# Kernel tuning notes

Hardware: AMD Instinct MI355X
Metric: run time of the kernel (lower is better)

The kernel has to match this reference:

```python
import jax, jax.numpy as jnp
import numpy as np

B, N, C, H = 2, 2048, 1024, 16
HD = C // H  # head dim = 64


def setup_inputs() -> dict:
    key = jax.random.key(0)
    kq, kk, kv, km = jax.random.split(key, 4)
    q = jax.random.normal(kq, (B, N, C), dtype=jnp.float32)
    k = jax.random.normal(kk, (B, N, C), dtype=jnp.float32)
    v = jax.random.normal(kv, (B, N, C), dtype=jnp.float32)
    mask = jax.random.randint(km, (B, 1, N, N), 0, 2, dtype=jnp.int32)
    return {"q": q, "k": k, "v": v, "mask": mask}


def reference(q, k, v, mask):
    b, n, c = q.shape
    # (B, N, C) -> (B, H, N, HD)
    qh = q.reshape(b, n, H, HD).transpose(0, 2, 1, 3)
    kh = k.reshape(b, n, H, HD).transpose(0, 2, 1, 3)
    vh = v.reshape(b, n, H, HD).transpose(0, 2, 1, 3)
    scale = 1.0 / jnp.sqrt(jnp.float32(HD))
    # scores: (B, H, N, N)
    scores = jnp.einsum("bhqd,bhkd->bhqk", qh, kh) * scale
    scores = jnp.where(mask == 0, jnp.float32(-1e9), scores)
    probs = jax.nn.softmax(scores, axis=-1)
    atten = jnp.einsum("bhqk,bhkd->bhqd", probs, vh)
    # (B, H, N, HD) -> (B, N, C)
    return atten.transpose(0, 2, 1, 3).reshape(b, n, c)
```

## Files before the change

### kernel.cpp

```cpp
#include <hip/hip_runtime.h>
#include <hip/hip_bf16.h>

#define B_ 2
#define N_ 2048
#define C_ 1024
#define H_ 16
#define HD_ 64

#define KT 64
#define NT (N_ / KT)
#define TILE_E 4096
#define PSTR 72
#define NW 8
#define QB 128

#define QBM 128

typedef short s16x8 __attribute__((ext_vector_type(8)));
typedef short s16x4 __attribute__((ext_vector_type(4)));
typedef float f32x4 __attribute__((ext_vector_type(4)));
typedef float f32x16 __attribute__((ext_vector_type(16)));

__device__ __forceinline__ s16x8 cvt8(float4 a, float4 b) {
    union { s16x8 v; __hip_bfloat162 h[4]; } u;
    u.h[0] = __float22bfloat162_rn(float2{a.x, a.y});
    u.h[1] = __float22bfloat162_rn(float2{a.z, a.w});
    u.h[2] = __float22bfloat162_rn(float2{b.x, b.y});
    u.h[3] = __float22bfloat162_rn(float2{b.z, b.w});
    return u.v;
}

__device__ __forceinline__ void gll16(const void* g, void* l) {
    __builtin_amdgcn_global_load_lds(
        (const __attribute__((address_space(1))) unsigned*)g,
        (__attribute__((address_space(3))) unsigned*)l, 16, 0, 0);
}

__global__ __launch_bounds__(256)
void pack_mask(const int* __restrict__ M, unsigned long long* __restrict__ bits) {
    const int gw   = (blockIdx.x * 256 + threadIdx.x) >> 6;
    const int lane = threadIdx.x & 63;
#pragma unroll
    for (int it = 0; it < 16; ++it) {
        const size_t wi = (size_t)gw * 16 + it;
        unsigned long long bal = __ballot(M[wi * 64 + lane] != 0);
        if (lane == 0) bits[wi] = bal;
    }
}

__global__ __launch_bounds__(256)
void prepass(const int* __restrict__ M, const float* __restrict__ K,
             const float* __restrict__ V, unsigned long long* __restrict__ bits,
             ushort* __restrict__ Kw, ushort* __restrict__ Vw) {
    const int bid = blockIdx.x;
    const int tid = threadIdx.x;
    if (bid < 2048) {
        const int gt = bid * 256 + tid;
        const int4* src = (const int4*)M + (size_t)gt * 4;
        unsigned r = 0;
#pragma unroll
        for (int c = 0; c < 4; ++c) {
            const int4 m4 = src[c];
            r |= (m4.x != 0 ? 1u : 0u) << (c * 4 + 0);
            r |= (m4.y != 0 ? 1u : 0u) << (c * 4 + 1);
            r |= (m4.z != 0 ? 1u : 0u) << (c * 4 + 2);
            r |= (m4.w != 0 ? 1u : 0u) << (c * 4 + 3);
        }
        ((ushort*)bits)[gt] = (ushort)r;
    } else if (bid < 4096) {
        const int gt = (bid - 2048) * 256 + tid;
        const int b  = gt >> 18;
        const int h  = (gt >> 14) & 15;
        const int n  = (gt >> 3) & 2047;
        const int db = gt & 7;
        const size_t src = (size_t)(b * N_ + n) * C_ + h * 64 + db * 8;
        float4 f0 = *(const float4*)(K + src);
        float4 f1 = *(const float4*)(K + src + 4);
        const int key = n & 63, kt = n >> 6;
        const int p = (key & 32) | ((key & 4) << 2) | ((key & 16) >> 1)
                    | ((key & 8) >> 1) | (key & 3);
        ushort* dst = Kw + (size_t)((b * H_ + h) * NT + kt) * TILE_E
                         + p * 64 + ((db ^ (p & 7)) * 8);
        *(s16x8*)dst = cvt8(f0, f1);
    } else {
        const int gt  = (bid - 4096) * 256 + tid;
        const int b   = gt >> 16;
        const int h   = (gt >> 12) & 15;
        const int kt  = (gt >> 7) & 31;
        const int kb4 = (gt >> 3) & 15;
        const int db  = gt & 7;
        const int key0 = kb4 * 4;
        float f[4][8];
#pragma unroll
        for (int i = 0; i < 4; ++i) {
            const size_t src = (size_t)(b * N_ + kt * 64 + key0 + i) * C_ + h * 64 + db * 8;
            *(float4*)&f[i][0] = *(const float4*)(V + src);
            *(float4*)&f[i][4] = *(const float4*)(V + src + 4);
        }
        ushort* tb = Vw + (size_t)((b * H_ + h) * NT + kt) * TILE_E;
#pragma unroll
        for (int j = 0; j < 8; ++j) {
            const int d = db * 8 + j;
            union { s16x4 v; __hip_bfloat162 h2[2]; } u;
            u.h2[0] = __float22bfloat162_rn(float2{f[0][j], f[1][j]});
            u.h2[1] = __float22bfloat162_rn(float2{f[2][j], f[3][j]});
            *(s16x4*)(tb + d * 64 + (((key0 >> 3) ^ (d & 7)) * 8) + (key0 & 7)) = u.v;
        }
    }
}

__global__ __launch_bounds__(256)
void mha_fwd(const float* __restrict__ Q, const ushort* __restrict__ Kw,
             const ushort* __restrict__ Vw, const unsigned* __restrict__ bits,
             float* __restrict__ O) {
    __shared__ ushort Kl[2][TILE_E];
    __shared__ ushort Vt[2][TILE_E];

    const int sid = blockIdx.x;
    const int jj  = sid >> 3;
    const int hb  = ((sid & 7) << 2) | (jj & 3);
    const int qt  = jj >> 2;
    const int h   = hb & 15;
    const int b   = hb >> 4;

    const int tid  = threadIdx.x;
    const int w    = tid >> 6;
    const int lane = tid & 63;
    const int rl   = lane & 31;
    const int hh   = lane >> 5;
    const int e3   = rl & 7;

    const size_t head_off = (size_t)b * N_ * C_ + (size_t)h * HD_;
    const int qb = qt * QBM + w * 32;

    const float qs = 0.125f * 1.44269504088896f;
    const size_t qoff = head_off + (size_t)(qb + rl) * C_ + hh * 8;
    s16x8 qa[4];
#pragma unroll
    for (int i = 0; i < 4; ++i) {
        float4 a = *(const float4*)(Q + qoff + i * 16);
        float4 c = *(const float4*)(Q + qoff + i * 16 + 4);
        a.x*=qs; a.y*=qs; a.z*=qs; a.w*=qs;
        c.x*=qs; c.y*=qs; c.z*=qs; c.w*=qs;
        qa[i] = cvt8(a, c);
    }

    s16x8 onesb;
#pragma unroll
    for (int i = 0; i < 8; ++i) onesb[i] = (short)0x3F80;

    f32x16 acc0, acc1, sum;
#pragma unroll
    for (int j = 0; j < 16; ++j) { acc0[j] = 0.f; acc1[j] = 0.f; sum[j] = 0.f; }

    const size_t tilebase = (size_t)((b * H_ + h) * NT) * TILE_E;
    const ushort* Kg = Kw + tilebase + (size_t)tid * 8;
    const ushort* Vg = Vw + tilebase + (size_t)tid * 8;

    const unsigned* mq = bits + ((size_t)b * N_ + qb + rl) * (N_ / 32);

    gll16(Kg,        &Kl[0][w * 512]);
    gll16(Kg + 2048, &Kl[0][w * 512 + 2048]);
    gll16(Vg,        &Vt[0][w * 512]);
    gll16(Vg + 2048, &Vt[0][w * 512 + 2048]);
    const ushort* Kg_pf = Kg + TILE_E;
    const ushort* Vg_pf = Vg + TILE_E;

    uint4 mw = *(const uint4*)mq;  mq += 4;

    for (int kt2 = 0; kt2 < NT; kt2 += 2) {
        const bool pf1 = (kt2 + 2 < NT);
        uint4 mw_nxt = mw;
        if (pf1) { mw_nxt = *(const uint4*)mq; }
        mq += 4;
#pragma unroll
        for (int u = 0; u < 2; ++u) {
            __syncthreads();
            if (u == 0 || pf1) {
                gll16(Kg_pf,        &Kl[1 - u][w * 512]);
                gll16(Kg_pf + 2048, &Kl[1 - u][w * 512 + 2048]);
                gll16(Vg_pf,        &Vt[1 - u][w * 512]);
                gll16(Vg_pf + 2048, &Vt[1 - u][w * 512 + 2048]);
                Kg_pf += TILE_E;  Vg_pf += TILE_E;
            }

            f32x16 z0, z1;
#pragma unroll
            for (int j = 0; j < 16; ++j) { z0[j] = 0.f; z1[j] = 0.f; }
            __builtin_amdgcn_s_setprio(1);
#pragma unroll
            for (int i = 0; i < 4; ++i) {
                const int cb = ((i << 1) | hh) ^ e3;
                s16x8 k0 = *(const s16x8*)(&Kl[u][rl * 64 + (cb << 3)]);
                s16x8 k1 = *(const s16x8*)(&Kl[u][(rl + 32) * 64 + (cb << 3)]);
                z0 = __builtin_amdgcn_mfma_f32_32x32x16_bf16(k0, qa[i], z0, 0, 0, 0);
                z1 = __builtin_amdgcn_mfma_f32_32x32x16_bf16(k1, qa[i], z1, 0, 0, 0);
            }
            __builtin_amdgcn_s_setprio(0);

            const unsigned g0 = (u ? mw.z : mw.x) >> (hh * 8);
            const unsigned g1 = (u ? mw.w : mw.y) >> (hh * 8);
            s16x8 pa[4];
            auto soft = [&](const f32x16& z, unsigned wg, s16x8& fA, s16x8& fB) {
                float p[16];
#pragma unroll
                for (int R = 0; R < 4; ++R) {
                    const int base = ((R & 1) << 4) + ((R >> 1) << 2);
#pragma unroll
                    for (int r = 0; r < 4; ++r)
                        p[4 * R + r] = __builtin_amdgcn_exp2f(
                            ((wg >> (base + r)) & 1u) ? z[4 * R + r] : -1e9f);
                }
                union { s16x8 v; __hip_bfloat162 h2[4]; } uA, uB;
                uA.h2[0] = __float22bfloat162_rn(float2{p[0], p[1]});
                uA.h2[1] = __float22bfloat162_rn(float2{p[2], p[3]});
                uA.h2[2] = __float22bfloat162_rn(float2{p[8], p[9]});
                uA.h2[3] = __float22bfloat162_rn(float2{p[10], p[11]});
                uB.h2[0] = __float22bfloat162_rn(float2{p[4], p[5]});
                uB.h2[1] = __float22bfloat162_rn(float2{p[6], p[7]});
                uB.h2[2] = __float22bfloat162_rn(float2{p[12], p[13]});
                uB.h2[3] = __float22bfloat162_rn(float2{p[14], p[15]});
                fA = uA.v;  fB = uB.v;
            };
            soft(z0, g0, pa[0], pa[1]);
            soft(z1, g1, pa[2], pa[3]);

            __builtin_amdgcn_s_setprio(1);
#pragma unroll
            for (int i = 0; i < 4; ++i) {
                const int cb = ((i << 1) | hh) ^ e3;
                s16x8 v0 = *(const s16x8*)(&Vt[u][rl * 64 + (cb << 3)]);
                s16x8 v1 = *(const s16x8*)(&Vt[u][(rl + 32) * 64 + (cb << 3)]);
                acc0 = __builtin_amdgcn_mfma_f32_32x32x16_bf16(pa[i], v0, acc0, 0, 0, 0);
                acc1 = __builtin_amdgcn_mfma_f32_32x32x16_bf16(pa[i], v1, acc1, 0, 0, 0);
                sum  = __builtin_amdgcn_mfma_f32_32x32x16_bf16(pa[i], onesb, sum, 0, 0, 0);
            }
            __builtin_amdgcn_s_setprio(0);
        }
        mw = mw_nxt;
    }

#pragma unroll
    for (int reg = 0; reg < 16; ++reg) {
        const int qrow = qb + (reg & 3) + ((reg >> 2) << 3) + (hh << 2);
        const float inv = 1.0f / sum[reg];
        const size_t ob = head_off + (size_t)qrow * C_;
        O[ob + rl]      = acc0[reg] * inv;
        O[ob + rl + 32] = acc1[reg] * inv;
    }
}

#define KSTR 72
#define VSTR 72
__global__ __launch_bounds__(512, 4)
void mha_fwd_fb(const float* __restrict__ Q, const float* __restrict__ K,
                const float* __restrict__ V, const unsigned* __restrict__ bits,
                float* __restrict__ O) {
    __shared__ ushort Kl[2][KT * KSTR];
    __shared__ ushort Vt[2][HD_ * VSTR];
    __shared__ ushort Pl[NW][16 * PSTR];
    const int qt = blockIdx.x, h = blockIdx.y, b = blockIdx.z, tid = threadIdx.x;
    const int w = tid >> 6, lane = tid & 63, l16 = lane & 15, quad = lane >> 4;
    const size_t head_off = (size_t)b * N_ * C_ + (size_t)h * HD_;
    const int qb = qt * QB + w * 16;
    const float qs = 0.125f * 1.44269504088896f;
    const size_t qoff = head_off + (size_t)(qb + l16) * C_ + quad * 8;
    float4 q0 = *(const float4*)(Q + qoff);
    float4 q1 = *(const float4*)(Q + qoff + 4);
    float4 q2 = *(const float4*)(Q + qoff + 32);
    float4 q3 = *(const float4*)(Q + qoff + 36);
    q0.x*=qs; q0.y*=qs; q0.z*=qs; q0.w*=qs;
    q1.x*=qs; q1.y*=qs; q1.z*=qs; q1.w*=qs;
    q2.x*=qs; q2.y*=qs; q2.z*=qs; q2.w*=qs;
    q3.x*=qs; q3.y*=qs; q3.z*=qs; q3.w*=qs;
    const s16x8 qa0 = cvt8(q0, q1);
    const s16x8 qa1 = cvt8(q2, q3);
    f32x4 acc[4];
#pragma unroll
    for (int c = 0; c < 4; ++c) acc[c] = f32x4{0.f, 0.f, 0.f, 0.f};
    float lsum = 0.f;
    const int skey = tid >> 3, sd0 = (tid & 7) * 8;
    const int kp = tid >> 4, vd0 = (tid & 15) * 4;
    const int vcol = 2 * (kp & 3) + ((((kp >> 2) ^ (vd0 >> 3)) & 7) << 3);
    const unsigned* brow = bits + ((size_t)b * N_ + qb + l16) * (N_ / 32);
    const float SHIFT = 16.0f;
    {
        const size_t kbase = head_off + (size_t)skey * C_ + sd0;
        float4 kA = *(const float4*)(K + kbase);
        float4 kB = *(const float4*)(K + kbase + 4);
        *(s16x8*)(&Kl[0][skey * KSTR + sd0]) = cvt8(kA, kB);
        const size_t vbase = head_off + (size_t)(2 * kp) * C_ + vd0;
        float4 vA = *(const float4*)(V + vbase);
        float4 vB = *(const float4*)(V + vbase + C_);
        const float* ap = (const float*)&vA;
        const float* bp = (const float*)&vB;
#pragma unroll
        for (int i = 0; i < 4; ++i) {
            __hip_bfloat162 pr = __float22bfloat162_rn(float2{ap[i], bp[i]});
            *(unsigned*)(&Vt[0][(vd0 + i) * VSTR + vcol]) = *(unsigned*)&pr;
        }
    }
    for (int kt = 0; kt < NT; ++kt) {
        const int cur = kt & 1;
        float4 kA, kB, vA, vB;
        const bool has_next = (kt + 1 < NT);
        if (has_next) {
            const size_t kbase = head_off + (size_t)((kt + 1) * KT + skey) * C_ + sd0;
            kA = *(const float4*)(K + kbase);
            kB = *(const float4*)(K + kbase + 4);
            const size_t vbase = head_off + (size_t)((kt + 1) * KT + 2 * kp) * C_ + vd0;
            vA = *(const float4*)(V + vbase);
            vB = *(const float4*)(V + vbase + C_);
        }
        const unsigned w0 = brow[2 * kt];
        const unsigned w1 = brow[2 * kt + 1];
        __syncthreads();
        f32x4 s[4];
#pragma unroll
        for (int t = 0; t < 4; ++t) {
            s16x8 kb0 = *(const s16x8*)(&Kl[cur][(t * 16 + l16) * KSTR + quad * 8]);
            s16x8 kb1 = *(const s16x8*)(&Kl[cur][(t * 16 + l16) * KSTR + quad * 8 + 32]);
            f32x4 z = {0.f, 0.f, 0.f, 0.f};
            z = __builtin_amdgcn_mfma_f32_16x16x32_bf16(kb0, qa0, z, 0, 0, 0);
            z = __builtin_amdgcn_mfma_f32_16x16x32_bf16(kb1, qa1, z, 0, 0, 0);
            s[t] = z;
        }
        const unsigned a0 = w0 >> (quad * 4);
        const unsigned a1 = w1 >> (quad * 4);
#pragma unroll
        for (int t = 0; t < 4; ++t) {
            const unsigned aw = (t < 2) ? a0 : a1;
            const int sh = (t & 1) * 16;
            float p0 = exp2f((((aw >> (sh + 0)) & 1u) ? s[t][0] : -1e9f) - SHIFT);
            float p1 = exp2f((((aw >> (sh + 1)) & 1u) ? s[t][1] : -1e9f) - SHIFT);
            float p2 = exp2f((((aw >> (sh + 2)) & 1u) ? s[t][2] : -1e9f) - SHIFT);
            float p3 = exp2f((((aw >> (sh + 3)) & 1u) ? s[t][3] : -1e9f) - SHIFT);
            lsum += (p0 + p1) + (p2 + p3);
            union { s16x4 v; __hip_bfloat162 h2[2]; } uu;
            uu.h2[0] = __float22bfloat162_rn(float2{p0, p1});
            uu.h2[1] = __float22bfloat162_rn(float2{p2, p3});
            *(s16x4*)(&Pl[w][l16 * PSTR + t * 16 + quad * 4]) = uu.v;
        }
#pragma unroll
        for (int half = 0; half < 2; ++half) {
            s16x8 pa = *(const s16x8*)(&Pl[w][l16 * PSTR + half * 32 + quad * 8]);
#pragma unroll
            for (int c = 0; c < 4; ++c) {
                const int dr = c * 16 + l16;
                const int blk = (half * 4 + quad) ^ ((dr >> 3) & 7);
                s16x8 vb = *(const s16x8*)(&Vt[cur][dr * VSTR + blk * 8]);
                acc[c] = __builtin_amdgcn_mfma_f32_16x16x32_bf16(pa, vb, acc[c], 0, 0, 0);
            }
        }
        if (has_next) {
            *(s16x8*)(&Kl[1 - cur][skey * KSTR + sd0]) = cvt8(kA, kB);
            const float* ap = (const float*)&vA;
            const float* bp = (const float*)&vB;
#pragma unroll
            for (int i = 0; i < 4; ++i) {
                __hip_bfloat162 pr = __float22bfloat162_rn(float2{ap[i], bp[i]});
                *(unsigned*)(&Vt[1 - cur][(vd0 + i) * VSTR + vcol]) = *(unsigned*)&pr;
            }
        }
    }
    lsum += __shfl_xor(lsum, 16);
    lsum += __shfl_xor(lsum, 32);
#pragma unroll
    for (int r = 0; r < 4; ++r) {
        const float inv = 1.0f / __shfl(lsum, quad * 4 + r);
        const size_t obase = head_off + (size_t)(qb + quad * 4 + r) * C_;
        O[obase + l16]      = acc[0][r] * inv;
        O[obase + l16 + 16] = acc[1][r] * inv;
        O[obase + l16 + 32] = acc[2][r] * inv;
        O[obase + l16 + 48] = acc[3][r] * inv;
    }
}

extern "C" void kernel_launch(void* const* d_in, const int* in_sizes, int n_in,
                              void* d_out, int out_size, void* d_ws, size_t ws_size,
                              hipStream_t stream) {
    const float* q = (const float*)d_in[0];
    const float* k = (const float*)d_in[1];
    const float* v = (const float*)d_in[2];
    const int*   m = (const int*)d_in[3];
    float*       o = (float*)d_out;

    const size_t BITS_BYTES = (size_t)B_ * N_ * N_ / 8;
    const size_t KV_BYTES   = (size_t)B_ * H_ * N_ * HD_ * 2;
    const size_t NEED       = BITS_BYTES + 2 * KV_BYTES;

    unsigned long long* bits = (unsigned long long*)d_ws;

    if (ws_size >= NEED) {
        ushort* kw = (ushort*)((char*)d_ws + BITS_BYTES);
        ushort* vw = (ushort*)((char*)d_ws + BITS_BYTES + KV_BYTES);
        hipLaunchKernelGGL(prepass, dim3(4608), dim3(256), 0, stream,
                           m, k, v, bits, kw, vw);
        hipLaunchKernelGGL(mha_fwd, dim3(512), dim3(256), 0, stream,
                           q, kw, vw, (const unsigned*)bits, o);
    } else {
        hipLaunchKernelGGL(pack_mask, dim3(2048), dim3(256), 0, stream, m, bits);
        dim3 grid(N_ / QB, H_, B_);
        hipLaunchKernelGGL(mha_fwd_fb, grid, dim3(512), 0, stream,
                           q, k, v, (const unsigned*)bits, o);
    }
}
```

Baseline: 167.5 us.

## Process two key tiles per barrier with double-buffered pairs of K/V tiles

The main loop now loads two K/V tiles (a 128-key chunk) into each of two LDS buffers and runs one __syncthreads per pair instead of one per tile. Both QK^T MFMA groups run before the softmax and PV steps, so the second tile's score MFMAs can overlap the first tile's exp work. This halves barrier count and lengthens the prefetch distance. In exchange LDS use doubles to 64 KB per block and four score accumulators raise register pressure, which may lower occupancy.

Measured after the change: 166.8 us. About the same (-0.4%).

```diff
diff --git a/kernel.cpp b/kernel.cpp
--- a/kernel.cpp
+++ b/kernel.cpp
@@ -113,8 +113,8 @@
 void mha_fwd(const float* __restrict__ Q, const ushort* __restrict__ Kw,
              const ushort* __restrict__ Vw, const unsigned* __restrict__ bits,
              float* __restrict__ O) {
-    __shared__ ushort Kl[2][TILE_E];
-    __shared__ ushort Vt[2][TILE_E];
+    __shared__ ushort Kl[2][2][TILE_E];
+    __shared__ ushort Vt[2][2][TILE_E];
 
     const int sid = blockIdx.x;
     const int jj  = sid >> 3;
@@ -159,84 +159,118 @@
 
     const unsigned* mq = bits + ((size_t)b * N_ + qb + rl) * (N_ / 32);
 
-    gll16(Kg,        &Kl[0][w * 512]);
-    gll16(Kg + 2048, &Kl[0][w * 512 + 2048]);
-    gll16(Vg,        &Vt[0][w * 512]);
-    gll16(Vg + 2048, &Vt[0][w * 512 + 2048]);
-    const ushort* Kg_pf = Kg + TILE_E;
-    const ushort* Vg_pf = Vg + TILE_E;
+#pragma unroll
+    for (int uu = 0; uu < 2; ++uu) {
+        gll16(Kg + uu * TILE_E,        &Kl[0][uu][w * 512]);
+        gll16(Kg + uu * TILE_E + 2048, &Kl[0][uu][w * 512 + 2048]);
+        gll16(Vg + uu * TILE_E,        &Vt[0][uu][w * 512]);
+        gll16(Vg + uu * TILE_E + 2048, &Vt[0][uu][w * 512 + 2048]);
+    }
+    const ushort* Kg_pf = Kg + 2 * TILE_E;
+    const ushort* Vg_pf = Vg + 2 * TILE_E;
 
     uint4 mw = *(const uint4*)mq;  mq += 4;
 
+    auto soft = [&](const f32x16& z, unsigned wg, s16x8& fA, s16x8& fB) {
+        float p[16];
+#pragma unroll
+        for (int R = 0; R < 4; ++R) {
+            const int base = ((R & 1) << 4) + ((R >> 1) << 2);
+#pragma unroll
+            for (int r = 0; r < 4; ++r)
+                p[4 * R + r] = __builtin_amdgcn_exp2f(
+                    ((wg >> (base + r)) & 1u) ? z[4 * R + r] : -1e9f);
+        }
+        union { s16x8 v; __hip_bfloat162 h2[4]; } uA, uB;
+        uA.h2[0] = __float22bfloat162_rn(float2{p[0], p[1]});
+        uA.h2[1] = __float22bfloat162_rn(float2{p[2], p[3]});
+        uA.h2[2] = __float22bfloat162_rn(float2{p[8], p[9]});
+        uA.h2[3] = __float22bfloat162_rn(float2{p[10], p[11]});
+        uB.h2[0] = __float22bfloat162_rn(float2{p[4], p[5]});
+        uB.h2[1] = __float22bfloat162_rn(float2{p[6], p[7]});
+        uB.h2[2] = __float22bfloat162_rn(float2{p[12], p[13]});
+        uB.h2[3] = __float22bfloat162_rn(float2{p[14], p[15]});
+        fA = uA.v;  fB = uB.v;
+    };
+
     for (int kt2 = 0; kt2 < NT; kt2 += 2) {
-        const bool pf1 = (kt2 + 2 < NT);
+        const int buf = (kt2 >> 1) & 1;
+        const bool pf = (kt2 + 2 < NT);
         uint4 mw_nxt = mw;
-        if (pf1) { mw_nxt = *(const uint4*)mq; }
+        if (pf) { mw_nxt = *(const uint4*)mq; }
         mq += 4;
-#pragma unroll
-        for (int u = 0; u < 2; ++u) {
-            __syncthreads();
-            if (u == 0 || pf1) {
-                gll16(Kg_pf,        &Kl[1 - u][w * 512]);
-                gll16(Kg_pf + 2048, &Kl[1 - u][w * 512 + 2048]);
-                gll16(Vg_pf,        &Vt[1 - u][w * 512]);
-                gll16(Vg_pf + 2048, &Vt[1 - u][w * 512 + 2048]);
-                Kg_pf += TILE_E;  Vg_pf += TILE_E;
+
+        __syncthreads();
+        if (pf) {
+#pragma unroll
+            for (int uu = 0; uu < 2; ++uu) {
+                gll16(Kg_pf + uu * TILE_E,        &Kl[buf ^ 1][uu][w * 512]);
+                gll16(Kg_pf + uu * TILE_E + 2048, &Kl[buf ^ 1][uu][w * 512 + 2048]);
+                gll16(Vg_pf + uu * TILE_E,        &Vt[buf ^ 1][uu][w * 512]);
+                gll16(Vg_pf + uu * TILE_E + 2048, &Vt[buf ^ 1][uu][w * 512 + 2048]);
             }
-
-            f32x16 z0, z1;
-#pragma unroll
-            for (int j = 0; j < 16; ++j) { z0[j] = 0.f; z1[j] = 0.f; }
-            __builtin_amdgcn_s_setprio(1);
-#pragma unroll
-            for (int i = 0; i < 4; ++i) {
-                const int cb = ((i << 1) | hh) ^ e3;
-                s16x8 k0 = *(const s16x8*)(&Kl[u][rl * 64 + (cb << 3)]);
-                s16x8 k1 = *(const s16x8*)(&Kl[u][(rl + 32) * 64 + (cb << 3)]);
-                z0 = __builtin_amdgcn_mfma_f32_32x32x16_bf16(k0, qa[i], z0, 0, 0, 0);
-                z1 = __builtin_amdgcn_mfma_f32_32x32x16_bf16(k1, qa[i], z1, 0, 0, 0);
-            }
-            __builtin_amdgcn_s_setprio(0);
-
-            const unsigned g0 = (u ? mw.z : mw.x) >> (hh * 8);
-            const unsigned g1 = (u ? mw.w : mw.y) >> (hh * 8);
-            s16x8 pa[4];
-            auto soft = [&](const f32x16& z, unsigned wg, s16x8& fA, s16x8& fB) {
-                float p[16];
-#pragma unroll
-                for (int R = 0; R < 4; ++R) {
-                    const int base = ((R & 1) << 4) + ((R >> 1) << 2);
-#pragma unroll
-                    for (int r = 0; r < 4; ++r)
-                        p[4 * R + r] = __builtin_amdgcn_exp2f(
-                            ((wg >> (base + r)) & 1u) ? z[4 * R + r] : -1e9f);
-                }
-                union { s16x8 v; __hip_bfloat162 h2[4]; } uA, uB;
-                uA.h2[0] = __float22bfloat162_rn(float2{p[0], p[1]});
-                uA.h2[1] = __float22bfloat162_rn(float2{p[2], p[3]});
-                uA.h2[2] = __float22bfloat162_rn(float2{p[8], p[9]});
-                uA.h2[3] = __float22bfloat162_rn(float2{p[10], p[11]});
-                uB.h2[0] = __float22bfloat162_rn(float2{p[4], p[5]});
-                uB.h2[1] = __float22bfloat162_rn(float2{p[6], p[7]});
-                uB.h2[2] = __float22bfloat162_rn(float2{p[12], p[13]});
-                uB.h2[3] = __float22bfloat162_rn(float2{p[14], p[15]});
-                fA = uA.v;  fB = uB.v;
-            };
-            soft(z0, g0, pa[0], pa[1]);
-            soft(z1, g1, pa[2], pa[3]);
-
-            __builtin_amdgcn_s_setprio(1);
-#pragma unroll
-            for (int i = 0; i < 4; ++i) {
-                const int cb = ((i << 1) | hh) ^ e3;
-                s16x8 v0 = *(const s16x8*)(&Vt[u][rl * 64 + (cb << 3)]);
-                s16x8 v1 = *(const s16x8*)(&Vt[u][(rl + 32) * 64 + (cb << 3)]);
-                acc0 = __builtin_amdgcn_mfma_f32_32x32x16_bf16(pa[i], v0, acc0, 0, 0, 0);
-                acc1 = __builtin_amdgcn_mfma_f32_32x32x16_bf16(pa[i], v1, acc1, 0, 0, 0);
-                sum  = __builtin_amdgcn_mfma_f32_32x32x16_bf16(pa[i], onesb, sum, 0, 0, 0);
-            }
-            __builtin_amdgcn_s_setprio(0);
-        }
+            Kg_pf += 2 * TILE_E;  Vg_pf += 2 * TILE_E;
+        }
+
+        const ushort* K0 = &Kl[buf][0][0];
+        const ushort* K1 = &Kl[buf][1][0];
+        const ushort* V0 = &Vt[buf][0][0];
+        const ushort* V1 = &Vt[buf][1][0];
+
+        f32x16 z0, z1, z2, z3;
+#pragma unroll
+        for (int j = 0; j < 16; ++j) { z0[j]=0.f; z1[j]=0.f; z2[j]=0.f; z3[j]=0.f; }
+        __builtin_amdgcn_s_setprio(1);
+#pragma unroll
+        for (int i = 0; i < 4; ++i) {
+            const int cb = ((i << 1) | hh) ^ e3;
+            s16x8 k0 = *(const s16x8*)(K0 + rl * 64 + (cb << 3));
+            s16x8 k1 = *(const s16x8*)(K0 + (rl + 32) * 64 + (cb << 3));
+            z0 = __builtin_amdgcn_mfma_f32_32x32x16_bf16(k0, qa[i], z0, 0, 0, 0);
+            z1 = __builtin_amdgcn_mfma_f32_32x32x16_bf16(k1, qa[i], z1, 0, 0, 0);
+        }
+#pragma unroll
+        for (int i = 0; i < 4; ++i) {
+            const int cb = ((i << 1) | hh) ^ e3;
+            s16x8 k0 = *(const s16x8*)(K1 + rl * 64 + (cb << 3));
+            s16x8 k1 = *(const s16x8*)(K1 + (rl + 32) * 64 + (cb << 3));
+            z2 = __builtin_amdgcn_mfma_f32_32x32x16_bf16(k0, qa[i], z2, 0, 0, 0);
+            z3 = __builtin_amdgcn_mfma_f32_32x32x16_bf16(k1, qa[i], z3, 0, 0, 0);
+        }
+        __builtin_amdgcn_s_setprio(0);
+
+        s16x8 pa0[4];
+        soft(z0, mw.x >> (hh * 8), pa0[0], pa0[1]);
+        soft(z1, mw.y >> (hh * 8), pa0[2], pa0[3]);
+
+        __builtin_amdgcn_s_setprio(1);
+#pragma unroll
+        for (int i = 0; i < 4; ++i) {
+            const int cb = ((i << 1) | hh) ^ e3;
+            s16x8 v0 = *(const s16x8*)(V0 + rl * 64 + (cb << 3));
+            s16x8 v1 = *(const s16x8*)(V0 + (rl + 32) * 64 + (cb << 3));
+            acc0 = __builtin_amdgcn_mfma_f32_32x32x16_bf16(pa0[i], v0, acc0, 0, 0, 0);
+            acc1 = __builtin_amdgcn_mfma_f32_32x32x16_bf16(pa0[i], v1, acc1, 0, 0, 0);
+            sum  = __builtin_amdgcn_mfma_f32_32x32x16_bf16(pa0[i], onesb, sum, 0, 0, 0);
+        }
+        __builtin_amdgcn_s_setprio(0);
+
+        s16x8 pa1[4];
+        soft(z2, mw.z >> (hh * 8), pa1[0], pa1[1]);
+        soft(z3, mw.w >> (hh * 8), pa1[2], pa1[3]);
+
+        __builtin_amdgcn_s_setprio(1);
+#pragma unroll
+        for (int i = 0; i < 4; ++i) {
+            const int cb = ((i << 1) | hh) ^ e3;
+            s16x8 v0 = *(const s16x8*)(V1 + rl * 64 + (cb << 3));
+            s16x8 v1 = *(const s16x8*)(V1 + (rl + 32) * 64 + (cb << 3));
+            acc0 = __builtin_amdgcn_mfma_f32_32x32x16_bf16(pa1[i], v0, acc0, 0, 0, 0);
+            acc1 = __builtin_amdgcn_mfma_f32_32x32x16_bf16(pa1[i], v1, acc1, 0, 0, 0);
+            sum  = __builtin_amdgcn_mfma_f32_32x32x16_bf16(pa1[i], onesb, sum, 0, 0, 0);
+        }
+        __builtin_amdgcn_s_setprio(0);
+
         mw = mw_nxt;
     }
 
```

## Split attention key range across two blocks with a combine kernel

Applied to the files above, without the earlier changes.

Adds a split-K (flash-decoding style) path: each query tile's key sequence is split into two halves handled by separate blocks (1024 blocks instead of 512), each writing unnormalized partial accumulators and row sums to workspace. A new combine kernel sums the two partials and normalizes. The aim is more parallelism and occupancy on the many CUs. The cost is extra global traffic for the fp32 partials and a third kernel launch. The path relies on no max subtraction, since scores are unnormalized exp2 values, so the partials can simply be added.

Measured after the change: 180.0 us. +7.5%, slower.

```diff
diff --git a/kernel.cpp b/kernel.cpp
--- a/kernel.cpp
+++ b/kernel.cpp
@@ -9,6 +9,7 @@
 
 #define KT 64
 #define NT (N_ / KT)
+#define NTS (NT / 2)
 #define TILE_E 4096
 #define PSTR 72
 #define NW 8
@@ -107,6 +108,178 @@
             *(s16x4*)(tb + d * 64 + (((key0 >> 3) ^ (d & 7)) * 8) + (key0 & 7)) = u.v;
         }
     }
+}
+
+__global__ __launch_bounds__(256, 4)
+void mha_fwd_sk(const float* __restrict__ Q, const ushort* __restrict__ Kw,
+                const ushort* __restrict__ Vw, const unsigned* __restrict__ bits,
+                float* __restrict__ accw, float* __restrict__ sumw) {
+    __shared__ ushort Kl[2][TILE_E];
+    __shared__ ushort Vt[2][TILE_E];
+
+    const int sid  = blockIdx.x;
+    const int xcd  = sid & 7;
+    const int rest = sid >> 3;
+    const int hb   = (xcd << 2) | (rest & 3);
+    const int qt   = (rest >> 2) & 15;
+    const int sp   = rest >> 6;
+    const int h    = hb & 15;
+    const int b    = hb >> 4;
+
+    const int tid  = threadIdx.x;
+    const int w    = tid >> 6;
+    const int lane = tid & 63;
+    const int rl   = lane & 31;
+    const int hh   = lane >> 5;
+    const int e3   = rl & 7;
+
+    const size_t head_off = (size_t)b * N_ * C_ + (size_t)h * HD_;
+    const int qb = qt * QBM + w * 32;
+
+    const float qs = 0.125f * 1.44269504088896f;
+    const size_t qoff = head_off + (size_t)(qb + rl) * C_ + hh * 8;
+    s16x8 qa[4];
+#pragma unroll
+    for (int i = 0; i < 4; ++i) {
+        float4 a = *(const float4*)(Q + qoff + i * 16);
+        float4 c = *(const float4*)(Q + qoff + i * 16 + 4);
+        a.x*=qs; a.y*=qs; a.z*=qs; a.w*=qs;
+        c.x*=qs; c.y*=qs; c.z*=qs; c.w*=qs;
+        qa[i] = cvt8(a, c);
+    }
+
+    s16x8 onesb;
+#pragma unroll
+    for (int i = 0; i < 8; ++i) onesb[i] = (short)0x3F80;
+
+    f32x16 acc0, acc1, sum;
+#pragma unroll
+    for (int j = 0; j < 16; ++j) { acc0[j] = 0.f; acc1[j] = 0.f; sum[j] = 0.f; }
+
+    const size_t tilebase = (size_t)((b * H_ + h) * NT + sp * NTS) * TILE_E;
+    const ushort* Kg = Kw + tilebase + (size_t)tid * 8;
+    const ushort* Vg = Vw + tilebase + (size_t)tid * 8;
+
+    const unsigned* mq = bits + ((size_t)b * N_ + qb + rl) * (N_ / 32) + sp * (NTS * 2);
+
+    gll16(Kg,        &Kl[0][w * 512]);
+    gll16(Kg + 2048, &Kl[0][w * 512 + 2048]);
+    gll16(Vg,        &Vt[0][w * 512]);
+    gll16(Vg + 2048, &Vt[0][w * 512 + 2048]);
+    const ushort* Kg_pf = Kg + TILE_E;
+    const ushort* Vg_pf = Vg + TILE_E;
+
+    uint4 mw = *(const uint4*)mq;  mq += 4;
+
+    auto soft = [&](const f32x16& z, unsigned wg, s16x8& fA, s16x8& fB) {
+        float p[16];
+#pragma unroll
+        for (int R = 0; R < 4; ++R) {
+            const int base = ((R & 1) << 4) + ((R >> 1) << 2);
+#pragma unroll
+            for (int r = 0; r < 4; ++r) {
+                const int bit = base + r;
+                const float e = __builtin_amdgcn_exp2f(z[4 * R + r]);
+                const unsigned m = (unsigned)((int)(wg << (31 - bit)) >> 31);
+                p[4 * R + r] = __uint_as_float(__float_as_uint(e) & m);
+            }
+        }
+        union { s16x8 v; __hip_bfloat162 h2[4]; } uA, uB;
+        uA.h2[0] = __float22bfloat162_rn(float2{p[0], p[1]});
+        uA.h2[1] = __float22bfloat162_rn(float2{p[2], p[3]});
+        uA.h2[2] = __float22bfloat162_rn(float2{p[8], p[9]});
+        uA.h2[3] = __float22bfloat162_rn(float2{p[10], p[11]});
+        uB.h2[0] = __float22bfloat162_rn(float2{p[4], p[5]});
+        uB.h2[1] = __float22bfloat162_rn(float2{p[6], p[7]});
+        uB.h2[2] = __float22bfloat162_rn(float2{p[12], p[13]});
+        uB.h2[3] = __float22bfloat162_rn(float2{p[14], p[15]});
+        fA = uA.v;  fB = uB.v;
+    };
+
+    for (int kt2 = 0; kt2 < NTS; kt2 += 2) {
+        const bool pf1 = (kt2 + 2 < NTS);
+        uint4 mw_nxt = mw;
+        if (pf1) { mw_nxt = *(const uint4*)mq; }
+        mq += 4;
+#pragma unroll
+        for (int u = 0; u < 2; ++u) {
+            __syncthreads();
+            if (u == 0 || pf1) {
+                gll16(Kg_pf,        &Kl[1 - u][w * 512]);
+                gll16(Kg_pf + 2048, &Kl[1 - u][w * 512 + 2048]);
+                gll16(Vg_pf,        &Vt[1 - u][w * 512]);
+                gll16(Vg_pf + 2048, &Vt[1 - u][w * 512 + 2048]);
+                Kg_pf += TILE_E;  Vg_pf += TILE_E;
+            }
+
+            f32x16 z0, z1;
+#pragma unroll
+            for (int j = 0; j < 16; ++j) { z0[j] = 0.f; z1[j] = 0.f; }
+            __builtin_amdgcn_s_setprio(1);
+#pragma unroll
+            for (int i = 0; i < 4; ++i) {
+                const int cb = ((i << 1) | hh) ^ e3;
+                s16x8 k0 = *(const s16x8*)(&Kl[u][rl * 64 + (cb << 3)]);
+                s16x8 k1 = *(const s16x8*)(&Kl[u][(rl + 32) * 64 + (cb << 3)]);
+                z0 = __builtin_amdgcn_mfma_f32_32x32x16_bf16(k0, qa[i], z0, 0, 0, 0);
+                z1 = __builtin_amdgcn_mfma_f32_32x32x16_bf16(k1, qa[i], z1, 0, 0, 0);
+            }
+            __builtin_amdgcn_s_setprio(0);
+
+            const unsigned g0 = (u ? mw.z : mw.x) >> (hh * 8);
+            const unsigned g1 = (u ? mw.w : mw.y) >> (hh * 8);
+            s16x8 pa[4];
+            soft(z0, g0, pa[0], pa[1]);
+            soft(z1, g1, pa[2], pa[3]);
+
+            __builtin_amdgcn_s_setprio(1);
+#pragma unroll
+            for (int i = 0; i < 4; ++i) {
+                const int cb = ((i << 1) | hh) ^ e3;
+                s16x8 v0 = *(const s16x8*)(&Vt[u][rl * 64 + (cb << 3)]);
+                s16x8 v1 = *(const s16x8*)(&Vt[u][(rl + 32) * 64 + (cb << 3)]);
+                acc0 = __builtin_amdgcn_mfma_f32_32x32x16_bf16(pa[i], v0, acc0, 0, 0, 0);
+                acc1 = __builtin_amdgcn_mfma_f32_32x32x16_bf16(pa[i], v1, acc1, 0, 0, 0);
+                sum  = __builtin_amdgcn_mfma_f32_32x32x16_bf16(pa[i], onesb, sum, 0, 0, 0);
+            }
+            __builtin_amdgcn_s_setprio(0);
+        }
+        mw = mw_nxt;
+    }
+
+    float* accS = accw + (size_t)sp * ((size_t)B_ * N_ * C_);
+    float* sumS = sumw + (size_t)sp * ((size_t)B_ * H_ * N_);
+#pragma unroll
+    for (int reg = 0; reg < 16; ++reg) {
+        const int qrow = qb + (reg & 3) + ((reg >> 2) << 3) + (hh << 2);
+        const size_t ob = head_off + (size_t)qrow * C_;
+        accS[ob + rl]      = acc0[reg];
+        accS[ob + rl + 32] = acc1[reg];
+        if (rl == 0)
+            sumS[(size_t)(b * H_ + h) * N_ + qrow] = sum[reg];
+    }
+}
+
+__global__ __launch_bounds__(256)
+void combine(const float* __restrict__ accw, const float* __restrict__ sumw,
+             float* __restrict__ O) {
+    const size_t i = (size_t)blockIdx.x * 256 + threadIdx.x;
+    const float4 a0 = ((const float4*)accw)[i];
+    const float4 a1 = ((const float4*)(accw + (size_t)B_ * N_ * C_))[i];
+    const size_t e = i * 4;
+    const int c = (int)(e & (C_ - 1));
+    const int n = (int)((e >> 10) & (N_ - 1));
+    const int b = (int)(e >> 21);
+    const int h = c >> 6;
+    const size_t si = (size_t)(b * H_ + h) * N_ + n;
+    const float s = sumw[si] + sumw[(size_t)B_ * H_ * N_ + si];
+    const float inv = 1.0f / s;
+    float4 o;
+    o.x = (a0.x + a1.x) * inv;
+    o.y = (a0.y + a1.y) * inv;
+    o.z = (a0.z + a1.z) * inv;
+    o.w = (a0.w + a1.w) * inv;
+    ((float4*)O)[i] = o;
 }
 
 __global__ __launch_bounds__(256)
@@ -387,11 +560,25 @@
 
     const size_t BITS_BYTES = (size_t)B_ * N_ * N_ / 8;
     const size_t KV_BYTES   = (size_t)B_ * H_ * N_ * HD_ * 2;
+    const size_t ACC_BYTES  = (size_t)B_ * N_ * C_ * 4;
+    const size_t SUM_BYTES  = (size_t)B_ * H_ * N_ * 4;
     const size_t NEED       = BITS_BYTES + 2 * KV_BYTES;
+    const size_t NEED2      = NEED + 2 * ACC_BYTES + 2 * SUM_BYTES;
 
     unsigned long long* bits = (unsigned long long*)d_ws;
 
-    if (ws_size >= NEED) {
+    if (ws_size >= NEED2) {
+        ushort* kw = (ushort*)((char*)d_ws + BITS_BYTES);
+        ushort* vw = (ushort*)((char*)d_ws + BITS_BYTES + KV_BYTES);
+        float* accw = (float*)((char*)d_ws + NEED);
+        float* sumw = (float*)((char*)d_ws + NEED + 2 * ACC_BYTES);
+        hipLaunchKernelGGL(prepass, dim3(4608), dim3(256), 0, stream,
+                           m, k, v, bits, kw, vw);
+        hipLaunchKernelGGL(mha_fwd_sk, dim3(1024), dim3(256), 0, stream,
+                           q, kw, vw, (const unsigned*)bits, accw, sumw);
+        hipLaunchKernelGGL(combine, dim3((B_ * N_ * C_ / 4) / 256), dim3(256),
+                           0, stream, accw, sumw, o);
+    } else if (ws_size >= NEED) {
         ushort* kw = (ushort*)((char*)d_ws + BITS_BYTES);
         ushort* vw = (ushort*)((char*)d_ws + BITS_BYTES + KV_BYTES);
         hipLaunchKernelGGL(prepass, dim3(4608), dim3(256), 0, stream,
```
